# Kernel tuning notes

Hardware: AMD Instinct MI355X
Metric: run time of the kernel (lower is better)

## Reference

```python
import jax, jax.numpy as jnp
import numpy as np
from jax.scipy.special import logsumexp

BS, SEQ, DM = 4, 4096, 1024
H, HD = 16, 64
BLK = 128
NB = SEQ // BLK          # 32 blocks
MAX_NB = 32
N_ITERS = 5
TEMP = 1.0
CLIP = 1.0


def setup_inputs() -> dict:
    key = jax.random.key(0)
    ks = jax.random.split(key, 12)
    s = 0.02
    return {
        'inputs_q': jax.random.normal(ks[0], (BS, SEQ, DM), jnp.float32),
        'wq': jax.random.normal(ks[1], (DM, H, HD), jnp.float32) * s,
        'bq': jnp.zeros((H, HD), jnp.float32),
        'wk': jax.random.normal(ks[2], (DM, H, HD), jnp.float32) * s,
        'bk': jnp.zeros((H, HD), jnp.float32),
        'wv': jax.random.normal(ks[3], (DM, H, HD), jnp.float32) * s,
        'bv': jnp.zeros((H, HD), jnp.float32),
        'w_sort': jax.random.normal(ks[4], (H, HD, MAX_NB), jnp.float32) * s,
        'b_sort': jnp.zeros((MAX_NB,), jnp.float32),
        'wo': jax.random.normal(ks[5], (H, HD, DM), jnp.float32) * s,
        'bo': jnp.zeros((DM,), jnp.float32),
    }


def sinkhorn_operator(log_alpha, n_iters=N_ITERS, temp=TEMP, clip=CLIP):
    # non-causal path of the original: iterative row/col log-normalization
    n = log_alpha.shape[1]
    la = jnp.reshape(log_alpha, (-1, n, n)) / temp
    for _ in range(n_iters):
        la = la - logsumexp(la, axis=2, keepdims=True)  # row normalize
        la = la - logsumexp(la, axis=1, keepdims=True)  # col normalize
    return jnp.exp(jnp.clip(la, -clip, clip))


def reference(inputs_q, wq, bq, wk, bk, wv, bv, w_sort, b_sort, wo, bo):
    bs, qlen, _ = inputs_q.shape
    nb = qlen // BLK
    # QKV projections: (bs, seq, H, HD)
    q = jnp.einsum('bsf,fhd->bshd', inputs_q, wq) + bq
    k = jnp.einsum('bsf,fhd->bshd', inputs_q, wk) + bk  # self-attention: inputs_kv = inputs_q
    v = jnp.einsum('bsf,fhd->bshd', inputs_q, wv) + bv
    # block reshape: (bs, nb, BLK, H, HD)
    qb = q.reshape(bs, nb, BLK, H, HD)
    kb = k.reshape(bs, nb, BLK, H, HD)
    vb = v.reshape(bs, nb, BLK, H, HD)
    # sort network: pool keys within block, project (H,HD)->MAX_NB
    sum_key = jnp.sum(kb, axis=2)                                   # (bs, nb, H, HD)
    sort_out = jnp.einsum('bnhd,hdm->bnm', sum_key, w_sort) + b_sort
    sort_mat = sort_out[:, :, :nb]                                  # (bs, nb, nb)
    perm = sinkhorn_operator(sort_mat)                              # (bs, nb, nb)
    # soft block sorting of keys/values
    sorted_k = jnp.einsum('bnm,bmshd->bnshd', perm, kb)
    sorted_v = jnp.einsum('bnm,bmshd->bnshd', perm, vb)
    # attend within each block to [local kv ; sorted kv]
    kcat = jnp.concatenate([kb, sorted_k], axis=2)                  # (bs, nb, 2BLK, H, HD)
    vcat = jnp.concatenate([vb, sorted_v], axis=2)
    scale = 1.0 / jnp.sqrt(jnp.float32(HD))
    logits = jnp.einsum('bnqhd,bnkhd->bnhqk', qb * scale, kcat)     # (bs, nb, H, BLK, 2BLK)
    w = jax.nn.softmax(logits, axis=-1)
    x = jnp.einsum('bnhqk,bnkhd->bnqhd', w, vcat)                   # (bs, nb, BLK, H, HD)
    x = x.reshape(bs, qlen, H, HD)
    return jnp.einsum('bshd,hdf->bsf', x, wo) + bo
```

## Files before the change

### kernel.cpp

```cpp
#include <hip/hip_runtime.h>
#include <stdint.h>

typedef short bf16x8 __attribute__((ext_vector_type(8)));
typedef float f32x4 __attribute__((ext_vector_type(4)));
typedef unsigned short u16;
typedef unsigned short u16x4 __attribute__((ext_vector_type(4)));

#define AS1 __attribute__((address_space(1)))
#define AS3 __attribute__((address_space(3)))

__device__ __forceinline__ void gll16(const void* g, void* l) {
  __builtin_amdgcn_global_load_lds((const AS1 uint32_t*)g, (AS3 uint32_t*)l, 16, 0, 0);
}

__device__ __forceinline__ f32x4 mfma16(bf16x8 a, bf16x8 b, f32x4 c) {
  return __builtin_amdgcn_mfma_f32_16x16x32_bf16(a, b, c, 0, 0, 0);
}

__device__ __forceinline__ u16 f2bf(float f) {
  union { float f; uint32_t u; } c; c.f = f;
  uint32_t r = c.u + 0x7FFFu + ((c.u >> 16) & 1u);
  return (u16)(r >> 16);
}
__device__ __forceinline__ float bf2f(u16 h) {
  union { uint32_t u; float f; } c; c.u = ((uint32_t)h) << 16; return c.f;
}

__global__ __launch_bounds__(256) void k_cast(const float* __restrict__ in, u16* __restrict__ out) {
  int i = (blockIdx.x * 256 + threadIdx.x) * 4;
  float4 v = *(const float4*)(in + i);
  u16x4 r; r.x = f2bf(v.x); r.y = f2bf(v.y); r.z = f2bf(v.z); r.w = f2bf(v.w);
  *(u16x4*)(out + i) = r;
}

__global__ __launch_bounds__(1024) void k_transpose4(
    const float* __restrict__ wq, const float* __restrict__ wk,
    const float* __restrict__ wv, const float* __restrict__ wo,
    u16* __restrict__ Wqkvt, u16* __restrict__ Wot) {
  __shared__ float t[32][33];
  const float* src; u16* dst;
  int z = blockIdx.z;
  if (z == 0)      { src = wq; dst = Wqkvt; }
  else if (z == 1) { src = wk; dst = Wqkvt + 1024 * 1024; }
  else if (z == 2) { src = wv; dst = Wqkvt + 2 * 1024 * 1024; }
  else             { src = wo; dst = Wot; }
  int tx = threadIdx.x, ty = threadIdx.y;
  t[ty][tx] = src[(size_t)(blockIdx.y * 32 + ty) * 1024 + blockIdx.x * 32 + tx];
  __syncthreads();
  dst[(size_t)(blockIdx.x * 32 + ty) * 1024 + blockIdx.y * 32 + tx] = f2bf(t[tx][ty]);
}

__device__ __forceinline__ void gemm256_loop(
    const u16* __restrict__ Ag, const u16* __restrict__ Bg,
    u16* lds, int m0, int n0, f32x4 (&acc)[8][4])
{
  const int tid = threadIdx.x, lane = tid & 63, w = tid >> 6;
  const int wm = w >> 2, wn = w & 3;
  const int l8 = lane >> 3, c7 = lane & 7;
  const int mm = lane & 15, quad = lane >> 4;
  const int ch0 = (quad ^ (mm & 7)) * 8;
  const int ch1 = ((quad ^ (mm & 7)) ^ 4) * 8;

  const u16* aSt = Ag + (size_t)(m0 + w * 8 + l8) * 1024 + (c7 ^ l8) * 8;
  const u16* bSt = Bg + (size_t)(n0 + w * 8 + l8) * 1024 + (c7 ^ l8) * 8;
  u16* ldsAw = lds + w * 512;
  u16* ldsBw = lds + 32768 + w * 512;
  const u16* aR0 = lds + (wm * 128 + mm) * 64 + ch0;
  const u16* aR1 = lds + (wm * 128 + mm) * 64 + ch1;
  const u16* bR0 = lds + 32768 + (wn * 64 + mm) * 64 + ch0;
  const u16* bR1 = lds + 32768 + (wn * 64 + mm) * 64 + ch1;

#define STA(q, kt, buf) gll16(aSt + (q) * 65536 + (kt) * 64, ldsAw + (buf) * 16384 + (q) * 4096)
#define STB(q, kt, buf) gll16(bSt + (q) * 65536 + (kt) * 64, ldsBw + (buf) * 16384 + (q) * 4096)

#define LDA(C, MH) do {                                                                  \
    _Pragma("unroll")                                                                    \
    for (int i = 0; i < 4; ++i) {                                                        \
      af[i][0] = *(const bf16x8*)(aR0 + (C) * 16384 + ((MH) * 64 + i * 16) * 64);        \
      af[i][1] = *(const bf16x8*)(aR1 + (C) * 16384 + ((MH) * 64 + i * 16) * 64);        \
    }                                                                                    \
  } while (0)
#define LDB(C, NH) do {                                                                  \
    _Pragma("unroll")                                                                    \
    for (int j = 0; j < 2; ++j) {                                                        \
      bf[j][0] = *(const bf16x8*)(bR0 + (C) * 16384 + ((NH) * 32 + j * 16) * 64);        \
      bf[j][1] = *(const bf16x8*)(bR1 + (C) * 16384 + ((NH) * 32 + j * 16) * 64);        \
    }                                                                                    \
  } while (0)
#define MMQ(MH, NH) do {                                                                 \
    __builtin_amdgcn_s_barrier();                                                        \
    asm volatile("s_waitcnt lgkmcnt(0)" ::: "memory");                                   \
    __builtin_amdgcn_sched_barrier(0);                                                   \
    __builtin_amdgcn_s_setprio(1);                                                       \
    _Pragma("unroll")                                                                    \
    for (int ks = 0; ks < 2; ++ks)                                                       \
      _Pragma("unroll")                                                                  \
      for (int i = 0; i < 4; ++i)                                                        \
        _Pragma("unroll")                                                                \
        for (int j = 0; j < 2; ++j)                                                      \
          acc[(MH) * 4 + i][(NH) * 2 + j] =                                              \
              mfma16(af[i][ks], bf[j][ks], acc[(MH) * 4 + i][(NH) * 2 + j]);             \
    __builtin_amdgcn_s_setprio(0);                                                       \
  } while (0)

#pragma unroll
  for (int i = 0; i < 8; ++i)
#pragma unroll
    for (int j = 0; j < 4; ++j) acc[i][j] = (f32x4){0.f, 0.f, 0.f, 0.f};

  STA(0, 0, 0); STA(1, 0, 0); STA(2, 0, 0); STA(3, 0, 0);
  STB(0, 0, 0); STB(1, 0, 0); STB(2, 0, 0); STB(3, 0, 0);
  STA(0, 1, 1); STA(2, 1, 1);
  asm volatile("s_waitcnt vmcnt(2)" ::: "memory");
  __builtin_amdgcn_s_barrier();

#pragma unroll 1
  for (int t = 0; t < 16; t += 2) {
    bf16x8 af[4][2]; bf16x8 bf[2][2];
    {
      const int t1 = t + 1, t2 = t + 2;
      const bool s2 = t2 < 16;
      LDA(0, 0); LDB(0, 0); STA(1, t1, 1); STA(3, t1, 1);
      MMQ(0, 0);
      __builtin_amdgcn_s_barrier();
      LDB(0, 1); STB(0, t1, 1); STB(1, t1, 1);
      MMQ(0, 1);
      __builtin_amdgcn_s_barrier();
      LDA(0, 1); STB(2, t1, 1); STB(3, t1, 1); if (s2) { STA(0, t2, 0); STA(2, t2, 0); }
      MMQ(1, 1);
      __builtin_amdgcn_s_barrier();
      LDB(0, 0);
      MMQ(1, 0);
      if (s2) asm volatile("s_waitcnt vmcnt(2)" ::: "memory");
      else    asm volatile("s_waitcnt vmcnt(0)" ::: "memory");
      __builtin_amdgcn_s_barrier();
    }
    {
      const int t2 = t + 2, t3 = t + 3;
      const bool s1 = t2 < 16, s2 = t3 < 16;
      LDA(1, 0); LDB(1, 0); if (s1) { STA(1, t2, 0); STA(3, t2, 0); }
      MMQ(0, 0);
      __builtin_amdgcn_s_barrier();
      LDB(1, 1); if (s1) { STB(0, t2, 0); STB(1, t2, 0); }
      MMQ(0, 1);
      __builtin_amdgcn_s_barrier();
      LDA(1, 1); if (s1) { STB(2, t2, 0); STB(3, t2, 0); } if (s2) { STA(0, t3, 1); STA(2, t3, 1); }
      MMQ(1, 1);
      __builtin_amdgcn_s_barrier();
      LDB(1, 0);
      MMQ(1, 0);
      if (s2)      asm volatile("s_waitcnt vmcnt(2)" ::: "memory");
      else if (s1) asm volatile("s_waitcnt vmcnt(0)" ::: "memory");
      __builtin_amdgcn_s_barrier();
    }
  }
#undef MMQ
#undef LDA
#undef LDB
#undef STA
#undef STB
}

__global__ __launch_bounds__(512, 2) void k_gemm_qkv(
    const u16* __restrict__ A, const u16* __restrict__ Bt,
    const float* __restrict__ bq, const float* __restrict__ bk, const float* __restrict__ bv,
    u16* __restrict__ Qb, u16* __restrict__ Kb, u16* __restrict__ Vbt, float* __restrict__ sumk)
{
  __shared__ __align__(16) u16 LDS[65536];
  const int m0 = blockIdx.y * 256, n0 = blockIdx.x * 256;
  f32x4 acc[8][4];
  gemm256_loop(A, Bt, LDS, m0, n0, acc);

  const int tid = threadIdx.x, lane = tid & 63, w = tid >> 6;
  const int wm = w >> 2, wn = w & 3;
  const int mm = lane & 15, quad = lane >> 4;
  const int sel = n0 >> 10;
  const float* bias = sel == 0 ? bq : (sel == 1 ? bk : bv);
  const float scl = sel == 0 ? 0.125f : 1.0f;

#pragma unroll
  for (int nf = 0; nf < 4; ++nf) {
    int ngl = n0 + wn * 64 + nf * 16 + mm;
    int nq = ngl & 1023;
    int h = nq >> 6, d = nq & 63;
    float bval = bias[nq];
#pragma unroll
    for (int mf = 0; mf < 8; ++mf)
#pragma unroll
      for (int r = 0; r < 4; ++r) {
        int mg = m0 + wm * 128 + mf * 16 + quad * 4 + r;
        int b_ = mg >> 12, s = mg & 4095;
        float v = (acc[mf][nf][r] + bval) * scl;
        if (sel == 0)      Qb [((size_t)(b_ * 16 + h) * 4096 + s) * 64 + d] = f2bf(v);
        else if (sel == 1) Kb [((size_t)(b_ * 16 + h) * 4096 + s) * 64 + d] = f2bf(v);
        else               Vbt[((size_t)(b_ * 16 + h) * 64 + d) * 4096 + s] = f2bf(v);
      }
  }

  if (sel == 1) {
#pragma unroll
    for (int nf = 0; nf < 4; ++nf) {
      float ssum = 0.f;
#pragma unroll
      for (int mf = 0; mf < 8; ++mf)
#pragma unroll
        for (int r = 0; r < 4; ++r) ssum += acc[mf][nf][r];
      ssum += __shfl_xor(ssum, 16);
      ssum += __shfl_xor(ssum, 32);
      if (quad == 0) {
        int colg = (n0 - 1024) + wn * 64 + nf * 16 + mm;
        int b_ = m0 >> 12, nb2 = ((m0 >> 7) & 31) + wm;
        sumk[(size_t)(b_ * 32 + nb2) * 1024 + colg] = ssum + 128.f * bias[colg];
      }
    }
  }
}

__global__ __launch_bounds__(512, 2) void k_gemm_out(
    const u16* __restrict__ A, const u16* __restrict__ Bt,
    const float* __restrict__ bo, float* __restrict__ out)
{
  __shared__ __align__(16) u16 LDS[65536];
  const int m0 = blockIdx.y * 256, n0 = blockIdx.x * 256;
  f32x4 acc[8][4];
  gemm256_loop(A, Bt, LDS, m0, n0, acc);

  const int tid = threadIdx.x, lane = tid & 63, w = tid >> 6;
  const int wm = w >> 2, wn = w & 3;
  const int mm = lane & 15, quad = lane >> 4;
#pragma unroll
  for (int nf = 0; nf < 4; ++nf) {
    int ng = n0 + wn * 64 + nf * 16 + mm;
    float bval = bo[ng];
#pragma unroll
    for (int mf = 0; mf < 8; ++mf)
#pragma unroll
      for (int r = 0; r < 4; ++r) {
        int mg = m0 + wm * 128 + mf * 16 + quad * 4 + r;
        out[(size_t)mg * 1024 + ng] = acc[mf][nf][r] + bval;
      }
  }
}

__global__ __launch_bounds__(256) void k_sortmm(const float* __restrict__ sumk, const float* __restrict__ wsort,
                                                const float* __restrict__ bsort, float* __restrict__ so) {
  __shared__ float red[256];
  int n = blockIdx.x, b = blockIdx.y, t = threadIdx.x;
  int m = t & 31, kp = t >> 5;
  const float* row = sumk + (size_t)(b * 32 + n) * 1024;
  float acc = 0.f;
  for (int c = kp * 128; c < kp * 128 + 128; ++c) acc += row[c] * wsort[c * 32 + m];
  red[t] = acc;
  __syncthreads();
  if (t < 32) {
    float s = bsort[t];
#pragma unroll
    for (int q = 0; q < 8; ++q) s += red[q * 32 + t];
    so[(size_t)(b * 32 + n) * 32 + t] = s;
  }
}

__global__ __launch_bounds__(32) void k_sinkhorn(const float* __restrict__ so, float* __restrict__ perm) {
  __shared__ float A[32][33];
  int b = blockIdx.x, t = threadIdx.x;
  for (int i = 0; i < 32; ++i) A[i][t] = so[(size_t)(b * 32 + i) * 32 + t];
  __syncthreads();
  for (int it = 0; it < 5; ++it) {
    {
      float mx = -1e30f;
      for (int j = 0; j < 32; ++j) mx = fmaxf(mx, A[t][j]);
      float s = 0.f;
      for (int j = 0; j < 32; ++j) s += __expf(A[t][j] - mx);
      float l = mx + __logf(s);
      for (int j = 0; j < 32; ++j) A[t][j] -= l;
    }
    __syncthreads();
    {
      float mx = -1e30f;
      for (int j = 0; j < 32; ++j) mx = fmaxf(mx, A[j][t]);
      float s = 0.f;
      for (int j = 0; j < 32; ++j) s += __expf(A[j][t] - mx);
      float l = mx + __logf(s);
      for (int j = 0; j < 32; ++j) A[j][t] -= l;
    }
    __syncthreads();
  }
  for (int i = 0; i < 32; ++i)
    perm[(size_t)(b * 32 + i) * 32 + t] = __expf(fminf(fmaxf(A[i][t], -1.f), 1.f));
}

__global__ __launch_bounds__(256) void k_mix(
    const u16* __restrict__ Kb, const u16* __restrict__ Vbt, const float* __restrict__ perm,
    u16* __restrict__ Ksort, u16* __restrict__ Vsort)
{
  __shared__ float P[32][32];
  int b = blockIdx.z, y = blockIdx.y, xg = blockIdx.x;
  int tid = threadIdx.x;
#pragma unroll
  for (int i = 0; i < 4; ++i) {
    int idx = i * 256 + tid;
    P[idx >> 5][idx & 31] = perm[b * 1024 + idx];
  }
  __syncthreads();
  if (y < 16) {
    int h = y;
    int ss = xg * 4 + (tid >> 6), d = tid & 63;
    const u16* Kg = Kb + (size_t)(b * 16 + h) * 262144;
    float xk[32];
#pragma unroll
    for (int m = 0; m < 32; ++m) xk[m] = bf2f(Kg[(size_t)(m * 128 + ss) * 64 + d]);
    size_t tbase = (size_t)((b * 16 + h) * 32) * 8192;
#pragma unroll
    for (int nn = 0; nn < 32; ++nn) {
      float sk = 0.f;
#pragma unroll
      for (int m4 = 0; m4 < 8; ++m4) {
        float4 pv = *(const float4*)&P[nn][m4 * 4];
        sk += pv.x * xk[m4 * 4 + 0] + pv.y * xk[m4 * 4 + 1] + pv.z * xk[m4 * 4 + 2] + pv.w * xk[m4 * 4 + 3];
      }
      Ksort[tbase + (size_t)nn * 8192 + ss * 64 + d] = f2bf(sk);
    }
  } else {
    int h = y - 16;
    int d = xg * 2 + (tid >> 7), ss = tid & 127;
    const u16* Vg = Vbt + ((size_t)(b * 16 + h) * 64 + d) * 4096;
    float xv[32];
#pragma unroll
    for (int m = 0; m < 32; ++m) xv[m] = bf2f(Vg[m * 128 + ss]);
    size_t tbase = (size_t)((b * 16 + h) * 32) * 8192;
#pragma unroll
    for (int nn = 0; nn < 32; ++nn) {
      float sv = 0.f;
#pragma unroll
      for (int m4 = 0; m4 < 8; ++m4) {
        float4 pv = *(const float4*)&P[nn][m4 * 4];
        sv += pv.x * xv[m4 * 4 + 0] + pv.y * xv[m4 * 4 + 1] + pv.z * xv[m4 * 4 + 2] + pv.w * xv[m4 * 4 + 3];
      }
      Vsort[tbase + (size_t)nn * 8192 + d * 128 + ss] = f2bf(sv);
    }
  }
}

__global__ __launch_bounds__(256, 2) void k_attn(
    const u16* __restrict__ Qb, const u16* __restrict__ Kb, const u16* __restrict__ Ksort,
    const u16* __restrict__ Vbt, const u16* __restrict__ Vsort, u16* __restrict__ X)
{
  __shared__ u16 Ks[16384];
  __shared__ u16 Vlo[8192];
  __shared__ u16 Vhi[8192];
  int tid = threadIdx.x, lane = tid & 63, w = tid >> 6;
  int n = blockIdx.x, h = blockIdx.y, b = blockIdx.z;
  size_t bh = (size_t)(b * 16 + h);
  size_t tileK = bh * 32 + n;

  {
    int l8 = lane >> 3, sl8 = lane & 7;
    const u16* Korig = Kb + (bh * 4096 + (size_t)n * 128) * 64;
    const u16* Ksrt  = Ksort + tileK * 8192;
#pragma unroll
    for (int c = 0; c < 8; ++c) {
      int cc = w * 8 + c;
      int r = cc * 8 + l8;
      int pk = sl8 ^ (r & 7);
      const u16* src = (cc < 16) ? (Korig + (size_t)r * 64 + pk * 8)
                                 : (Ksrt + (size_t)(r - 128) * 64 + pk * 8);
      gll16(src, Ks + cc * 512);
    }
    int l16 = lane >> 4, sl16 = lane & 15;
    const u16* Vorig = Vbt + bh * 262144 + (size_t)n * 128;
    const u16* Vsrt  = Vsort + tileK * 8192;
#pragma unroll
    for (int c = 0; c < 4; ++c) {
      int cc = w * 4 + c;
      int d = cc * 4 + l16;
      int pv = sl16 ^ (d & 15);
      gll16(Vorig + (size_t)d * 4096 + pv * 8, Vlo + cc * 512);
      gll16(Vsrt + (size_t)d * 128 + pv * 8, Vhi + cc * 512);
    }
  }

  int mm = lane & 15, quad = lane >> 4;
  bf16x8 qf[2][2];
  {
    size_t qrow = bh * 4096 + n * 128 + w * 32;
#pragma unroll
    for (int mt = 0; mt < 2; ++mt)
#pragma unroll
      for (int ks = 0; ks < 2; ++ks)
        qf[mt][ks] = *(const bf16x8*)(Qb + (qrow + mt * 16 + mm) * 64 + ks * 32 + quad * 8);
  }
  __syncthreads();

  f32x4 S[2][16];
#pragma unroll
  for (int mt = 0; mt < 2; ++mt)
#pragma unroll
    for (int nt = 0; nt < 16; ++nt) S[mt][nt] = (f32x4){0.f, 0.f, 0.f, 0.f};
#pragma unroll
  for (int nt = 0; nt < 16; ++nt) {
    int kk = nt * 16 + mm;
#pragma unroll
    for (int ks = 0; ks < 2; ++ks) {
      int ch = (ks * 4 + quad) ^ (kk & 7);
      bf16x8 bk = *(const bf16x8*)(Ks + kk * 64 + ch * 8);
      S[0][nt] = mfma16(qf[0][ks], bk, S[0][nt]);
      S[1][nt] = mfma16(qf[1][ks], bk, S[1][nt]);
    }
  }

  float mx[2][4], ls[2][4];
#pragma unroll
  for (int mt = 0; mt < 2; ++mt)
#pragma unroll
    for (int r = 0; r < 4; ++r) {
      float v = S[mt][0][r];
#pragma unroll
      for (int nt = 1; nt < 16; ++nt) v = fmaxf(v, S[mt][nt][r]);
#pragma unroll
      for (int o = 1; o < 16; o <<= 1) v = fmaxf(v, __shfl_xor(v, o));
      mx[mt][r] = v;
    }
#pragma unroll
  for (int mt = 0; mt < 2; ++mt)
#pragma unroll
    for (int nt = 0; nt < 16; ++nt)
#pragma unroll
      for (int r = 0; r < 4; ++r)
        S[mt][nt][r] = __expf(S[mt][nt][r] - mx[mt][r]);
#pragma unroll
  for (int mt = 0; mt < 2; ++mt)
#pragma unroll
    for (int r = 0; r < 4; ++r) {
      float s = 0.f;
#pragma unroll
      for (int nt = 0; nt < 16; ++nt) s += S[mt][nt][r];
#pragma unroll
      for (int o = 1; o < 16; o <<= 1) s += __shfl_xor(s, o);
      ls[mt][r] = s;
    }

  __syncthreads();

  u16* Pw = Ks + w * 4096;
  f32x4 O[2][4];
#pragma unroll
  for (int mt = 0; mt < 2; ++mt)
#pragma unroll
    for (int dt = 0; dt < 4; ++dt) O[mt][dt] = (f32x4){0.f, 0.f, 0.f, 0.f};

#pragma unroll
  for (int half = 0; half < 2; ++half) {
    const u16* Vp = half == 0 ? Vlo : Vhi;
#pragma unroll
    for (int mt = 0; mt < 2; ++mt)
#pragma unroll
      for (int nt8 = 0; nt8 < 8; ++nt8) {
        int nt = half * 8 + nt8;
        int kkl = nt8 * 16 + mm;
#pragma unroll
        for (int r = 0; r < 4; ++r) {
          int q = mt * 16 + quad * 4 + r;
          int ch = (kkl >> 3) ^ (q & 15);
          Pw[q * 128 + ch * 8 + (kkl & 7)] = f2bf(S[mt][nt][r]);
        }
      }
#pragma unroll
    for (int ksl = 0; ksl < 4; ++ksl) {
      bf16x8 pa[2];
#pragma unroll
      for (int mt = 0; mt < 2; ++mt) {
        int q = mt * 16 + mm;
        int ch = (ksl * 4 + quad) ^ (q & 15);
        pa[mt] = *(const bf16x8*)(Pw + q * 128 + ch * 8);
      }
#pragma unroll
      for (int dt = 0; dt < 4; ++dt) {
        int d = dt * 16 + mm;
        int ch = (ksl * 4 + quad) ^ (d & 15);
        bf16x8 vb = *(const bf16x8*)(Vp + d * 128 + ch * 8);
        O[0][dt] = mfma16(pa[0], vb, O[0][dt]);
        O[1][dt] = mfma16(pa[1], vb, O[1][dt]);
      }
    }
  }

#pragma unroll
  for (int mt = 0; mt < 2; ++mt)
#pragma unroll
    for (int dt = 0; dt < 4; ++dt)
#pragma unroll
      for (int r = 0; r < 4; ++r) {
        int q = w * 32 + mt * 16 + quad * 4 + r;
        float val = O[mt][dt][r] / ls[mt][r];
        size_t row = (size_t)b * 4096 + n * 128 + q;
        X[row * 1024 + h * 64 + dt * 16 + mm] = f2bf(val);
      }
}

extern "C" void kernel_launch(void* const* d_in, const int* in_sizes, int n_in,
                              void* d_out, int out_size, void* d_ws, size_t ws_size,
                              hipStream_t stream) {
  const float* inq   = (const float*)d_in[0];
  const float* wq    = (const float*)d_in[1];
  const float* bq    = (const float*)d_in[2];
  const float* wk    = (const float*)d_in[3];
  const float* bk    = (const float*)d_in[4];
  const float* wv    = (const float*)d_in[5];
  const float* bv    = (const float*)d_in[6];
  const float* wsort = (const float*)d_in[7];
  const float* bsort = (const float*)d_in[8];
  const float* wo    = (const float*)d_in[9];
  const float* bo    = (const float*)d_in[10];
  float* out = (float*)d_out;

  char* ws = (char*)d_ws;
  size_t off = 0;
  auto alloc = [&](size_t bytes) { char* p = ws + off; off += (bytes + 255) & ~(size_t)255; return p; };
  u16*  Qb    = (u16*)alloc(33554432);
  u16*  Kb    = (u16*)alloc(33554432);
  u16*  Vbt   = (u16*)alloc(33554432);
  u16*  Ksort = (u16*)alloc(33554432);
  u16*  Vsort = (u16*)alloc(33554432);
  u16*  Abf   = (u16*)alloc(33554432);
  u16*  Wqkvt = (u16*)alloc(6291456);
  u16*  Wot   = (u16*)alloc(2097152);
  float* sumk = (float*)alloc(524288);
  float* so   = (float*)alloc(16384);
  float* perm = (float*)alloc(16384);
  u16*  X = Abf;

  k_cast<<<16384, 256, 0, stream>>>(inq, Abf);
  k_transpose4<<<dim3(32, 32, 4), dim3(32, 32), 0, stream>>>(wq, wk, wv, wo, Wqkvt, Wot);
  k_gemm_qkv<<<dim3(12, 64), 512, 0, stream>>>(Abf, Wqkvt, bq, bk, bv, Qb, Kb, Vbt, sumk);
  k_sortmm<<<dim3(32, 4), 256, 0, stream>>>(sumk, wsort, bsort, so);
  k_sinkhorn<<<4, 32, 0, stream>>>(so, perm);
  k_mix<<<dim3(32, 32, 4), 256, 0, stream>>>(Kb, Vbt, perm, Ksort, Vsort);
  k_attn<<<dim3(32, 16, 4), 256, 0, stream>>>(Qb, Kb, Ksort, Vbt, Vsort, X);
  k_gemm_out<<<dim3(4, 64), 512, 0, stream>>>(X, Wot, bo, out);
}
```

Baseline: 495.3 us.

## Deepen GEMM prefetch, remap blocks across XCDs, and transpose V stores via LDS

```diff
diff --git a/kernel.cpp b/kernel.cpp
--- a/kernel.cpp
+++ b/kernel.cpp
@@ -103,6 +103,26 @@
     __builtin_amdgcn_s_setprio(0);                                                       \
   } while (0)
 
+#define TILE(TT, C) do {                                                                 \
+    const int t1 = (TT) + 1, t2 = (TT) + 2;                                              \
+    const bool sB = t1 < 16, sA = t2 < 16;                                               \
+    LDA(C, 0); LDB(C, 0); if (sB) { STB(0, t1, 1 - (C)); STB(1, t1, 1 - (C)); }          \
+    MMQ(0, 0);                                                                           \
+    __builtin_amdgcn_s_barrier();                                                        \
+    LDB(C, 1); if (sB) { STB(2, t1, 1 - (C)); STB(3, t1, 1 - (C)); }                     \
+    if (sA) { STA(0, t2, C); STA(2, t2, C); }                                            \
+    MMQ(0, 1);                                                                           \
+    __builtin_amdgcn_s_barrier();                                                        \
+    LDA(C, 1);                                                                           \
+    MMQ(1, 1);                                                                           \
+    __builtin_amdgcn_s_barrier();                                                        \
+    LDB(C, 0); if (sA) { STA(1, t2, C); STA(3, t2, C); }                                 \
+    MMQ(1, 0);                                                                           \
+    if ((TT) < 14)       asm volatile("s_waitcnt vmcnt(4)" ::: "memory");                \
+    else if ((TT) == 14) asm volatile("s_waitcnt vmcnt(0)" ::: "memory");                \
+    __builtin_amdgcn_s_barrier();                                                        \
+  } while (0)
+
 #pragma unroll
   for (int i = 0; i < 8; ++i)
 #pragma unroll
@@ -110,50 +130,17 @@
 
   STA(0, 0, 0); STA(1, 0, 0); STA(2, 0, 0); STA(3, 0, 0);
   STB(0, 0, 0); STB(1, 0, 0); STB(2, 0, 0); STB(3, 0, 0);
-  STA(0, 1, 1); STA(2, 1, 1);
-  asm volatile("s_waitcnt vmcnt(2)" ::: "memory");
+  STA(0, 1, 1); STA(1, 1, 1); STA(2, 1, 1); STA(3, 1, 1);
+  asm volatile("s_waitcnt vmcnt(4)" ::: "memory");
   __builtin_amdgcn_s_barrier();
 
 #pragma unroll 1
   for (int t = 0; t < 16; t += 2) {
     bf16x8 af[4][2]; bf16x8 bf[2][2];
-    {
-      const int t1 = t + 1, t2 = t + 2;
-      const bool s2 = t2 < 16;
-      LDA(0, 0); LDB(0, 0); STA(1, t1, 1); STA(3, t1, 1);
-      MMQ(0, 0);
-      __builtin_amdgcn_s_barrier();
-      LDB(0, 1); STB(0, t1, 1); STB(1, t1, 1);
-      MMQ(0, 1);
-      __builtin_amdgcn_s_barrier();
-      LDA(0, 1); STB(2, t1, 1); STB(3, t1, 1); if (s2) { STA(0, t2, 0); STA(2, t2, 0); }
-      MMQ(1, 1);
-      __builtin_amdgcn_s_barrier();
-      LDB(0, 0);
-      MMQ(1, 0);
-      if (s2) asm volatile("s_waitcnt vmcnt(2)" ::: "memory");
-      else    asm volatile("s_waitcnt vmcnt(0)" ::: "memory");
-      __builtin_amdgcn_s_barrier();
-    }
-    {
-      const int t2 = t + 2, t3 = t + 3;
-      const bool s1 = t2 < 16, s2 = t3 < 16;
-      LDA(1, 0); LDB(1, 0); if (s1) { STA(1, t2, 0); STA(3, t2, 0); }
-      MMQ(0, 0);
-      __builtin_amdgcn_s_barrier();
-      LDB(1, 1); if (s1) { STB(0, t2, 0); STB(1, t2, 0); }
-      MMQ(0, 1);
-      __builtin_amdgcn_s_barrier();
-      LDA(1, 1); if (s1) { STB(2, t2, 0); STB(3, t2, 0); } if (s2) { STA(0, t3, 1); STA(2, t3, 1); }
-      MMQ(1, 1);
-      __builtin_amdgcn_s_barrier();
-      LDB(1, 0);
-      MMQ(1, 0);
-      if (s2)      asm volatile("s_waitcnt vmcnt(2)" ::: "memory");
-      else if (s1) asm volatile("s_waitcnt vmcnt(0)" ::: "memory");
-      __builtin_amdgcn_s_barrier();
-    }
-  }
+    TILE(t, 0);
+    TILE(t + 1, 1);
+  }
+#undef TILE
 #undef MMQ
 #undef LDA
 #undef LDB
@@ -167,7 +154,9 @@
     u16* __restrict__ Qb, u16* __restrict__ Kb, u16* __restrict__ Vbt, float* __restrict__ sumk)
 {
   __shared__ __align__(16) u16 LDS[65536];
-  const int m0 = blockIdx.y * 256, n0 = blockIdx.x * 256;
+  int lin = blockIdx.x + 12 * blockIdx.y;
+  int nb = (lin & 7) * 96 + (lin >> 3);
+  const int m0 = (nb / 12) * 256, n0 = (nb % 12) * 256;
   f32x4 acc[8][4];
   gemm256_loop(A, Bt, LDS, m0, n0, acc);
 
@@ -176,8 +165,39 @@
   const int mm = lane & 15, quad = lane >> 4;
   const int sel = n0 >> 10;
   const float* bias = sel == 0 ? bq : (sel == 1 ? bk : bv);
+
+  if (sel == 2) {
+    u16* W = LDS + w * 8192;
+#pragma unroll
+    for (int nf = 0; nf < 4; ++nf) {
+      int d = nf * 16 + mm;
+      float bval = bias[((n0 & 1023) + wn * 64 + nf * 16 + mm)];
+#pragma unroll
+      for (int mf = 0; mf < 8; ++mf) {
+        int c = mf * 4 + quad;
+        u16x4 pk;
+        pk.x = f2bf(acc[mf][nf][0] + bval);
+        pk.y = f2bf(acc[mf][nf][1] + bval);
+        pk.z = f2bf(acc[mf][nf][2] + bval);
+        pk.w = f2bf(acc[mf][nf][3] + bval);
+        *(u16x4*)(W + d * 128 + (c ^ (d & 15)) * 4) = pk;
+      }
+    }
+    asm volatile("s_waitcnt lgkmcnt(0)" ::: "memory");
+    int h_w = ((n0 & 1023) >> 6) + wn;
+    int b_ = m0 >> 12;
+    int c = lane & 31, dpar = lane >> 5;
+    size_t gbase = ((size_t)(b_ * 16 + h_w) * 64) * 4096 + (m0 & 4095) + wm * 128 + c * 4;
+#pragma unroll
+    for (int dd = 0; dd < 32; ++dd) {
+      int d = dd * 2 + dpar;
+      u16x4 v = *(const u16x4*)(W + d * 128 + (c ^ (d & 15)) * 4);
+      *(u16x4*)(Vbt + gbase + (size_t)d * 4096) = v;
+    }
+    return;
+  }
+
   const float scl = sel == 0 ? 0.125f : 1.0f;
-
 #pragma unroll
   for (int nf = 0; nf < 4; ++nf) {
     int ngl = n0 + wn * 64 + nf * 16 + mm;
@@ -191,9 +211,8 @@
         int mg = m0 + wm * 128 + mf * 16 + quad * 4 + r;
         int b_ = mg >> 12, s = mg & 4095;
         float v = (acc[mf][nf][r] + bval) * scl;
-        if (sel == 0)      Qb [((size_t)(b_ * 16 + h) * 4096 + s) * 64 + d] = f2bf(v);
-        else if (sel == 1) Kb [((size_t)(b_ * 16 + h) * 4096 + s) * 64 + d] = f2bf(v);
-        else               Vbt[((size_t)(b_ * 16 + h) * 64 + d) * 4096 + s] = f2bf(v);
+        if (sel == 0) Qb[((size_t)(b_ * 16 + h) * 4096 + s) * 64 + d] = f2bf(v);
+        else          Kb[((size_t)(b_ * 16 + h) * 4096 + s) * 64 + d] = f2bf(v);
       }
   }
 
@@ -221,7 +240,9 @@
     const float* __restrict__ bo, float* __restrict__ out)
 {
   __shared__ __align__(16) u16 LDS[65536];
-  const int m0 = blockIdx.y * 256, n0 = blockIdx.x * 256;
+  int lin = blockIdx.x + 4 * blockIdx.y;
+  int nb = (lin & 7) * 32 + (lin >> 3);
+  const int m0 = (nb / 4) * 256, n0 = (nb % 4) * 256;
   f32x4 acc[8][4];
   gemm256_loop(A, Bt, LDS, m0, n0, acc);
 
```

Result: faster. 446.9 us (-9.8%).
